# Kernel tuning notes

Measured on AMD Instinct MI355X. Metric: run time of the kernel, lower is better.

## Reference

```python
import jax, jax.numpy as jnp
import numpy as np

HIDDEN = 1024
HEADS = 16
HEAD = HIDDEN // HEADS
B, S = 2, 2048


def setup_inputs() -> dict:
    key = jax.random.key(0)
    ks = jax.random.split(key, 8)
    query = jax.random.normal(ks[0], (B, S, HIDDEN), dtype=jnp.float32)
    key_t = jax.random.normal(ks[1], (B, S, HIDDEN), dtype=jnp.float32)
    value = jax.random.normal(ks[2], (B, S, HIDDEN), dtype=jnp.float32)
    # causal mask, broadcastable over batch and heads; 0 -> masked (-inf)
    mask = jnp.tril(jnp.ones((S, S), dtype=jnp.int32))[None, None, :, :]
    # torch Linear weights are [out_features, in_features]
    scale = 0.02
    Wq = jax.random.normal(ks[3], (HIDDEN, HIDDEN), dtype=jnp.float32) * scale
    Wk = jax.random.normal(ks[4], (HIDDEN, HIDDEN), dtype=jnp.float32) * scale
    Wv = jax.random.normal(ks[5], (HIDDEN, HIDDEN), dtype=jnp.float32) * scale
    Wo = jax.random.normal(ks[6], (HIDDEN, HIDDEN), dtype=jnp.float32) * scale
    bo = jax.random.normal(ks[7], (HIDDEN,), dtype=jnp.float32) * scale
    return {"query": query, "key": key_t, "value": value, "mask": mask,
            "Wq": Wq, "Wk": Wk, "Wv": Wv, "Wo": Wo, "bo": bo}


def reference(query, key, value, mask, Wq, Wk, Wv, Wo, bo):
    b = query.shape[0]
    # Linear (no bias): x @ W^T, then split into heads -> [b, h, s, d]
    def heads(x, W):
        y = jnp.einsum('bse,oe->bso', x, W)
        return y.reshape(b, -1, HEADS, HEAD).transpose(0, 2, 1, 3)
    Q = heads(query, Wq)
    K = heads(key, Wk)
    V = heads(value, Wv)
    inv_scale = 1.0 / jnp.sqrt(jnp.float32(HEAD))
    scores = jnp.einsum('bhqd,bhkd->bhqk', Q, K) * inv_scale  # [b,h,s,s]
    scores = jnp.where(mask == 0, -jnp.inf, scores)
    attn = jax.nn.softmax(scores, axis=-1)
    x = jnp.einsum('bhqk,bhkd->bhqd', attn, V)
    x = x.transpose(0, 2, 1, 3).reshape(b, -1, HIDDEN)
    return jnp.einsum('bse,oe->bso', x, Wo) + bo
```

## Files before the change

kernel.cpp:

```cpp
#include <hip/hip_runtime.h>


typedef __attribute__((ext_vector_type(8))) short short8;
typedef __attribute__((ext_vector_type(4))) float f32x4;
typedef unsigned int u32;
typedef unsigned short u16;

__device__ inline f32x4 mfma16(short8 a, short8 b, f32x4 c) {
    return __builtin_amdgcn_mfma_f32_16x16x32_bf16(a, b, c, 0, 0, 0);
}
__device__ inline u16 f2bf(float f) {
    union { float f; u32 u; } v; v.f = f;
    u32 r = v.u + 0x7fff + ((v.u >> 16) & 1);
    return (u16)(r >> 16);
}
__device__ inline void gll16(void* lds, const void* g) {
    __builtin_amdgcn_global_load_lds((const __attribute__((address_space(1))) u32*)g,
                                     (__attribute__((address_space(3))) u32*)lds,
                                     16, 0, 0);
}
__device__ inline u32 pkbf(float hi, float lo) {
    return __builtin_amdgcn_perm(__float_as_uint(hi), __float_as_uint(lo),
                                 0x07060302u);
}

__global__ __launch_bounds__(256)
void cvt_all(const float* __restrict__ q, const float* __restrict__ k,
             const float* __restrict__ v, const float* __restrict__ wq,
             const float* __restrict__ wk, const float* __restrict__ wv,
             const float* __restrict__ wo,
             u16* __restrict__ q16, u16* __restrict__ k16,
             u16* __restrict__ v16, u16* __restrict__ w16) {
    const size_t QKV = 1u << 22;
    const size_t WSZ = 1u << 20;
    size_t base = ((size_t)blockIdx.x * 256 + threadIdx.x) * 8;
    const float* src; u16* dst; size_t off; float scale = 1.0f;
    if (base < QKV)            { src = q; dst = q16; off = base;
                                 scale = 0.125f * 1.44269504f; }
    else if (base < 2 * QKV)   { src = k; dst = k16; off = base - QKV;     }
    else if (base < 3 * QKV)   { src = v; dst = v16; off = base - 2 * QKV; }
    else {
        size_t wb = base - 3 * QKV;
        int wi = (int)(wb >> 20); off = wb & (WSZ - 1);
        src = wi == 0 ? wq : wi == 1 ? wk : wi == 2 ? wv : wo;
        dst = w16 + (size_t)wi * WSZ;
    }
    float4 f0 = *(const float4*)(src + off);
    float4 f1 = *(const float4*)(src + off + 4);
    short8 s = { (short)f2bf(f0.x * scale), (short)f2bf(f0.y * scale),
                 (short)f2bf(f0.z * scale), (short)f2bf(f0.w * scale),
                 (short)f2bf(f1.x * scale), (short)f2bf(f1.y * scale),
                 (short)f2bf(f1.z * scale), (short)f2bf(f1.w * scale) };
    *(short8*)(dst + off) = s;
}

__global__ __launch_bounds__(256)
void gemm_qkv(const u16* __restrict__ q16, const u16* __restrict__ k16,
              const u16* __restrict__ v16, const u16* __restrict__ w16,
              u16* __restrict__ Qg, u16* __restrict__ Kg, u16* __restrict__ Vt) {
    const int K = 1024;
    __shared__ u16 As[2][128 * 32];
    __shared__ u16 Bs[2][128 * 32];
    const int z = blockIdx.z;
    const u16* A = z == 0 ? q16 : z == 1 ? k16 : v16;
    const u16* W = w16 + (size_t)z * (1u << 20);

    const int tid = threadIdx.x, lane = tid & 63, w = tid >> 6;
    const int ln15 = lane & 15, quad = lane >> 4;
    const int fr = (ln15 >> 1) & 3;
    const int lrow = lane >> 2;
    const int lcs = (((lane & 3) ^ ((lane >> 3) & 3)) << 3);
    const int m0 = blockIdx.y * 128, n0 = blockIdx.x * 128;
    const int wm = (w >> 1) * 64, wn = (w & 1) * 64;

    f32x4 acc[4][4] = {};

    #pragma unroll
    for (int c = 0; c < 2; ++c) {
        gll16(&As[0][(w * 32 + c * 16) * 32],
              &A[(size_t)(m0 + w * 32 + c * 16 + lrow) * K + lcs]);
        gll16(&Bs[0][(w * 32 + c * 16) * 32],
              &W[(size_t)(n0 + w * 32 + c * 16 + lrow) * K + lcs]);
    }

    for (int i = 0; i < 32; ++i) {
        const int cur = i & 1, nb = cur ^ 1;
        __asm__ volatile("s_waitcnt vmcnt(0)" ::: "memory");
        __builtin_amdgcn_s_barrier();
        __builtin_amdgcn_sched_barrier(0);

        if (i < 31) {
            const int k0 = (i + 1) * 32;
            #pragma unroll
            for (int c = 0; c < 2; ++c) {
                gll16(&As[nb][(w * 32 + c * 16) * 32],
                      &A[(size_t)(m0 + w * 32 + c * 16 + lrow) * K + k0 + lcs]);
                gll16(&Bs[nb][(w * 32 + c * 16) * 32],
                      &W[(size_t)(n0 + w * 32 + c * 16 + lrow) * K + k0 + lcs]);
            }
        }
        __builtin_amdgcn_sched_barrier(0);

        short8 a[4], b[4];
        #pragma unroll
        for (int mt = 0; mt < 4; ++mt)
            a[mt] = *(const short8*)&As[cur][(wm + mt * 16 + ln15) * 32 +
                                            ((quad ^ fr) << 3)];
        #pragma unroll
        for (int nt = 0; nt < 4; ++nt)
            b[nt] = *(const short8*)&Bs[cur][(wn + nt * 16 + ln15) * 32 +
                                            ((quad ^ fr) << 3)];
        #pragma unroll
        for (int mt = 0; mt < 4; ++mt)
            #pragma unroll
            for (int nt = 0; nt < 4; ++nt)
                acc[mt][nt] = mfma16(a[mt], b[nt], acc[mt][nt]);
    }

    #pragma unroll
    for (int mt = 0; mt < 4; ++mt)
        #pragma unroll
        for (int nt = 0; nt < 4; ++nt)
            #pragma unroll
            for (int r = 0; r < 4; ++r) {
                int m = m0 + wm + mt * 16 + quad * 4 + r;
                int n = n0 + wn + nt * 16 + ln15;
                u16 hv = f2bf(acc[mt][nt][r]);
                if (z == 2) {
                    int b_ = m >> 11, s_ = m & 2047, h_ = n >> 6, d_ = n & 63;
                    int kl = s_ & 63;
                    int sp = (s_ & ~63) + (kl & 15) * 4 + (kl >> 4);
                    Vt[((size_t)(b_ * 16 + h_) * 64 + d_) * 2048 + sp] = hv;
                } else {
                    u16* dst = z ? Kg : Qg;
                    dst[(size_t)m * 1024 + n] = hv;
                }
            }
}

__global__ __launch_bounds__(256)
void gemm_out(const u16* __restrict__ A, const u16* __restrict__ W,
              const float* __restrict__ bias, float* __restrict__ out) {
    const int K = 1024;
    __shared__ u16 As[2][64 * 64];
    __shared__ u16 Bs[2][128 * 64];
    const int id = blockIdx.x;
    const int by = id >> 3, bx = id & 7;

    const int tid = threadIdx.x, lane = tid & 63, w = tid >> 6;
    const int ln15 = lane & 15, quad = lane >> 4, s7 = ln15 & 7;
    const int lr = lane >> 3;
    const int lcs = (((lane & 7) ^ lr) << 3);
    const int m0 = by * 64, n0 = bx * 128;
    const int wm = (w & 1) * 32, wn = (w >> 1) * 64;

    f32x4 acc[2][4] = {};

    #pragma unroll
    for (int c = 0; c < 2; ++c)
        gll16(&As[0][(w * 16 + c * 8) * 64],
              &A[(size_t)(m0 + w * 16 + c * 8 + lr) * K + lcs]);
    #pragma unroll
    for (int c = 0; c < 4; ++c)
        gll16(&Bs[0][(w * 32 + c * 8) * 64],
              &W[(size_t)(n0 + w * 32 + c * 8 + lr) * K + lcs]);

    for (int i = 0; i < 16; ++i) {
        const int cur = i & 1, nb = cur ^ 1;
        __asm__ volatile("s_waitcnt vmcnt(0)" ::: "memory");
        __builtin_amdgcn_s_barrier();
        __builtin_amdgcn_sched_barrier(0);

        if (i < 15) {
            const int k0 = (i + 1) * 64;
            #pragma unroll
            for (int c = 0; c < 2; ++c)
                gll16(&As[nb][(w * 16 + c * 8) * 64],
                      &A[(size_t)(m0 + w * 16 + c * 8 + lr) * K + k0 + lcs]);
            #pragma unroll
            for (int c = 0; c < 4; ++c)
                gll16(&Bs[nb][(w * 32 + c * 8) * 64],
                      &W[(size_t)(n0 + w * 32 + c * 8 + lr) * K + k0 + lcs]);
        }
        __builtin_amdgcn_sched_barrier(0);

        #pragma unroll
        for (int kh = 0; kh < 2; ++kh) {
            short8 a[2], b[4];
            #pragma unroll
            for (int mt = 0; mt < 2; ++mt)
                a[mt] = *(const short8*)&As[cur][(wm + mt * 16 + ln15) * 64 +
                                                (((kh * 4 + quad) ^ s7) << 3)];
            #pragma unroll
            for (int nt = 0; nt < 4; ++nt)
                b[nt] = *(const short8*)&Bs[cur][(wn + nt * 16 + ln15) * 64 +
                                                (((kh * 4 + quad) ^ s7) << 3)];
            #pragma unroll
            for (int mt = 0; mt < 2; ++mt)
                #pragma unroll
                for (int nt = 0; nt < 4; ++nt)
                    acc[mt][nt] = mfma16(a[mt], b[nt], acc[mt][nt]);
        }
    }

    #pragma unroll
    for (int mt = 0; mt < 2; ++mt)
        #pragma unroll
        for (int nt = 0; nt < 4; ++nt)
            #pragma unroll
            for (int r = 0; r < 4; ++r) {
                int m = m0 + wm + mt * 16 + quad * 4 + r;
                int n = n0 + wn + nt * 16 + ln15;
                out[(size_t)m * 1024 + n] = acc[mt][nt][r] + bias[n];
            }
}

__global__ __launch_bounds__(256)
void attn3(const u16* __restrict__ Qg, const u16* __restrict__ Kg,
           const u16* __restrict__ Vt, u16* __restrict__ Xb) {
    __shared__ u16 Kl[2][64 * 64];
    __shared__ u16 Vl[2][64 * 64];
    __shared__ u16 Pl[4][16 * 72];

    const int id = blockIdx.x;
    const int bh = id & 31, qt = 31 - (id >> 5);
    const int b = bh >> 4, h = bh & 15;
    const int tid = threadIdx.x, lane = tid & 63, w = tid >> 6;
    const int ln15 = lane & 15, quad = lane >> 4, s7 = ln15 & 7;
    const int lr = lane >> 3;
    const int lcs = (((lane & 7) ^ lr) << 3);
    const u16* Kbase = Kg + (size_t)b * 2048 * 1024 + h * 64;
    const u16* Vbase = Vt + (size_t)bh * 64 * 2048;
    const float M0L = 8.65617025f;
    const int q0 = qt * 64;

    const u16* qrow = Qg + (size_t)(b * 2048 + q0 + w * 16 + ln15) * 1024 + h * 64;
    short8 aq0 = *(const short8*)(qrow + quad * 8);
    short8 aq1 = *(const short8*)(qrow + 32 + quad * 8);
    __asm__ volatile("s_waitcnt vmcnt(0)" ::: "memory");

    f32x4 o[4] = {};
    float lsum[4] = {0.f, 0.f, 0.f, 0.f};

    #pragma unroll
    for (int c = 0; c < 2; ++c) {
        const int r0 = w * 16 + c * 8;
        gll16(&Kl[0][r0 * 64], Kbase + (size_t)(r0 + lr) * 1024 + lcs);
        gll16(&Vl[0][r0 * 64], Vbase + (size_t)(r0 + lr) * 2048 + lcs);
    }

    for (int kt = 0; kt <= qt; ++kt) {
        const int cur = kt & 1, nb = cur ^ 1;
        __asm__ volatile("s_waitcnt vmcnt(0)" ::: "memory");
        __builtin_amdgcn_s_barrier();
        __builtin_amdgcn_sched_barrier(0);

        if (kt < qt) {
            const int nk = (kt + 1) * 64;
            #pragma unroll
            for (int c = 0; c < 2; ++c) {
                const int r0 = w * 16 + c * 8;
                gll16(&Kl[nb][r0 * 64], Kbase + (size_t)(nk + r0 + lr) * 1024 + lcs);
                gll16(&Vl[nb][r0 * 64], Vbase + (size_t)(r0 + lr) * 2048 + nk + lcs);
            }
        }
        __builtin_amdgcn_sched_barrier(0);

        f32x4 sc[4];
        #pragma unroll
        for (int ct = 0; ct < 4; ++ct) {
            short8 b0 = *(const short8*)&Kl[cur][(ct * 16 + ln15) * 64 +
                                                ((quad ^ s7) << 3)];
            short8 b1 = *(const short8*)&Kl[cur][(ct * 16 + ln15) * 64 +
                                                (((4 + quad) ^ s7) << 3)];
            f32x4 c = {};
            c = mfma16(aq0, b0, c);
            c = mfma16(aq1, b1, c);
            sc[ct] = c;
        }

        const bool diag = (kt == qt);
        #pragma unroll
        for (int r = 0; r < 4; ++r) {
            float s0 = sc[0][r], s1 = sc[1][r], s2 = sc[2][r], s3 = sc[3][r];
            if (diag) {
                const int qq = w * 16 + quad * 4 + r;
                s0 = (ln15      <= qq) ? s0 : -1e30f;
                s1 = (16 + ln15 <= qq) ? s1 : -1e30f;
                s2 = (32 + ln15 <= qq) ? s2 : -1e30f;
                s3 = (48 + ln15 <= qq) ? s3 : -1e30f;
            }
            float p0 = __builtin_amdgcn_exp2f(s0 - M0L);
            float p1 = __builtin_amdgcn_exp2f(s1 - M0L);
            float p2 = __builtin_amdgcn_exp2f(s2 - M0L);
            float p3 = __builtin_amdgcn_exp2f(s3 - M0L);
            uint2 pw = make_uint2(pkbf(p1, p0), pkbf(p3, p2));
            *(uint2*)&Pl[w][(quad * 4 + r) * 72 + ln15 * 4] = pw;
            lsum[r] += (p0 + p1) + (p2 + p3);
        }

        __asm__ volatile("s_waitcnt lgkmcnt(0)" ::: "memory");
        short8 ap0 = *(const short8*)&Pl[w][ln15 * 72 + quad * 8];
        short8 ap1 = *(const short8*)&Pl[w][ln15 * 72 + 32 + quad * 8];

        #pragma unroll
        for (int dt = 0; dt < 4; ++dt) {
            short8 bv0 = *(const short8*)&Vl[cur][(dt * 16 + ln15) * 64 +
                                                 ((quad ^ s7) << 3)];
            short8 bv1 = *(const short8*)&Vl[cur][(dt * 16 + ln15) * 64 +
                                                 (((4 + quad) ^ s7) << 3)];
            o[dt] = mfma16(ap0, bv0, o[dt]);
            o[dt] = mfma16(ap1, bv1, o[dt]);
        }
    }

    #pragma unroll
    for (int r = 0; r < 4; ++r) {
        float l = lsum[r];
        #pragma unroll
        for (int off = 1; off < 16; off <<= 1)
            l += __shfl_xor(l, off);
        lsum[r] = l;
    }
    #pragma unroll
    for (int dt = 0; dt < 4; ++dt)
        #pragma unroll
        for (int r = 0; r < 4; ++r) {
            int q = q0 + w * 16 + quad * 4 + r;
            Xb[(size_t)(b * 2048 + q) * 1024 + h * 64 + dt * 16 + ln15] =
                f2bf(o[dt][r] / lsum[r]);
        }
}

extern "C" void kernel_launch(void* const* d_in, const int* in_sizes, int n_in,
                              void* d_out, int out_size, void* d_ws, size_t ws_size,
                              hipStream_t stream) {
    const float* query = (const float*)d_in[0];
    const float* key   = (const float*)d_in[1];
    const float* value = (const float*)d_in[2];
    const float* Wq = (const float*)d_in[4];
    const float* Wk = (const float*)d_in[5];
    const float* Wv = (const float*)d_in[6];
    const float* Wo = (const float*)d_in[7];
    const float* bo = (const float*)d_in[8];
    float* out = (float*)d_out;

    u16* ws  = (u16*)d_ws;
    const size_t T = 1ull << 22;
    u16* q16 = ws;
    u16* k16 = ws + T;
    u16* v16 = ws + 2 * T;
    u16* w16 = ws + 3 * T;
    u16* Qg  = ws + 4 * T;
    u16* Kg  = ws + 5 * T;
    u16* Vt  = (u16*)d_out;
    u16* Xb  = q16;
    const size_t WSZ = 1ull << 20;

    cvt_all<<<8192, 256, 0, stream>>>(query, key, value, Wq, Wk, Wv, Wo,
                                      q16, k16, v16, w16);

    gemm_qkv<<<dim3(8, 32, 3), 256, 0, stream>>>(q16, k16, v16, w16, Qg, Kg, Vt);

    attn3<<<1024, 256, 0, stream>>>(Qg, Kg, Vt, Xb);

    gemm_out<<<512, 256, 0, stream>>>(Xb, w16 + 3 * WSZ, bo, out);
}
```

Baseline: 222.5 us.

## Triple-buffer LDS tiles in QKV, output GEMM and attention kernels

Switches the LDS staging in all three main kernels from double to triple buffering with prefetch distance two. The wait changes from vmcnt(0) to a partial vmcnt, so only the current tile's loads must finish before the barrier while the next tile's loads stay in flight. The intent is to hide more global-load latency behind the MFMA work. It costs 50% more LDS for the K/V and A/B tiles, which may reduce occupancy, and adds ring-index bookkeeping.

Measured after the change: 223.3 us. About the same (+0.3%).

```diff
diff --git a/kernel.cpp b/kernel.cpp
--- a/kernel.cpp
+++ b/kernel.cpp
@@ -59,8 +59,8 @@
               const u16* __restrict__ v16, const u16* __restrict__ w16,
               u16* __restrict__ Qg, u16* __restrict__ Kg, u16* __restrict__ Vt) {
     const int K = 1024;
-    __shared__ u16 As[2][128 * 32];
-    __shared__ u16 Bs[2][128 * 32];
+    __shared__ u16 As[3][128 * 32];
+    __shared__ u16 Bs[3][128 * 32];
     const int z = blockIdx.z;
     const u16* A = z == 0 ? q16 : z == 1 ? k16 : v16;
     const u16* W = w16 + (size_t)z * (1u << 20);
@@ -76,21 +76,28 @@
     f32x4 acc[4][4] = {};
 
     #pragma unroll
-    for (int c = 0; c < 2; ++c) {
-        gll16(&As[0][(w * 32 + c * 16) * 32],
-              &A[(size_t)(m0 + w * 32 + c * 16 + lrow) * K + lcs]);
-        gll16(&Bs[0][(w * 32 + c * 16) * 32],
-              &W[(size_t)(n0 + w * 32 + c * 16 + lrow) * K + lcs]);
-    }
-
-    for (int i = 0; i < 32; ++i) {
-        const int cur = i & 1, nb = cur ^ 1;
-        __asm__ volatile("s_waitcnt vmcnt(0)" ::: "memory");
+    for (int t = 0; t < 2; ++t)
+        #pragma unroll
+        for (int c = 0; c < 2; ++c) {
+            gll16(&As[t][(w * 32 + c * 16) * 32],
+                  &A[(size_t)(m0 + w * 32 + c * 16 + lrow) * K + t * 32 + lcs]);
+            gll16(&Bs[t][(w * 32 + c * 16) * 32],
+                  &W[(size_t)(n0 + w * 32 + c * 16 + lrow) * K + t * 32 + lcs]);
+        }
+
+    int cur = 0;
+    for (int t = 0; t < 32; ++t) {
+        if (t < 31) {
+            __asm__ volatile("s_waitcnt vmcnt(4)" ::: "memory");
+        } else {
+            __asm__ volatile("s_waitcnt vmcnt(0)" ::: "memory");
+        }
         __builtin_amdgcn_s_barrier();
         __builtin_amdgcn_sched_barrier(0);
 
-        if (i < 31) {
-            const int k0 = (i + 1) * 32;
+        if (t < 30) {
+            const int k0 = (t + 2) * 32;
+            const int nb = (cur + 2 >= 3) ? cur - 1 : cur + 2;
             #pragma unroll
             for (int c = 0; c < 2; ++c) {
                 gll16(&As[nb][(w * 32 + c * 16) * 32],
@@ -115,6 +122,8 @@
             #pragma unroll
             for (int nt = 0; nt < 4; ++nt)
                 acc[mt][nt] = mfma16(a[mt], b[nt], acc[mt][nt]);
+
+        cur = (cur == 2) ? 0 : cur + 1;
     }
 
     #pragma unroll
@@ -142,8 +151,8 @@
 void gemm_out(const u16* __restrict__ A, const u16* __restrict__ W,
               const float* __restrict__ bias, float* __restrict__ out) {
     const int K = 1024;
-    __shared__ u16 As[2][64 * 64];
-    __shared__ u16 Bs[2][128 * 64];
+    __shared__ u16 As[3][64 * 64];
+    __shared__ u16 Bs[3][128 * 64];
     const int id = blockIdx.x;
     const int by = id >> 3, bx = id & 7;
 
@@ -157,22 +166,30 @@
     f32x4 acc[2][4] = {};
 
     #pragma unroll
-    for (int c = 0; c < 2; ++c)
-        gll16(&As[0][(w * 16 + c * 8) * 64],
-              &A[(size_t)(m0 + w * 16 + c * 8 + lr) * K + lcs]);
-    #pragma unroll
-    for (int c = 0; c < 4; ++c)
-        gll16(&Bs[0][(w * 32 + c * 8) * 64],
-              &W[(size_t)(n0 + w * 32 + c * 8 + lr) * K + lcs]);
-
+    for (int t = 0; t < 2; ++t) {
+        #pragma unroll
+        for (int c = 0; c < 2; ++c)
+            gll16(&As[t][(w * 16 + c * 8) * 64],
+                  &A[(size_t)(m0 + w * 16 + c * 8 + lr) * K + t * 64 + lcs]);
+        #pragma unroll
+        for (int c = 0; c < 4; ++c)
+            gll16(&Bs[t][(w * 32 + c * 8) * 64],
+                  &W[(size_t)(n0 + w * 32 + c * 8 + lr) * K + t * 64 + lcs]);
+    }
+
+    int cur = 0;
     for (int i = 0; i < 16; ++i) {
-        const int cur = i & 1, nb = cur ^ 1;
-        __asm__ volatile("s_waitcnt vmcnt(0)" ::: "memory");
+        if (i < 15) {
+            __asm__ volatile("s_waitcnt vmcnt(6)" ::: "memory");
+        } else {
+            __asm__ volatile("s_waitcnt vmcnt(0)" ::: "memory");
+        }
         __builtin_amdgcn_s_barrier();
         __builtin_amdgcn_sched_barrier(0);
 
-        if (i < 15) {
-            const int k0 = (i + 1) * 64;
+        if (i < 14) {
+            const int k0 = (i + 2) * 64;
+            const int nb = (cur + 2 >= 3) ? cur - 1 : cur + 2;
             #pragma unroll
             for (int c = 0; c < 2; ++c)
                 gll16(&As[nb][(w * 16 + c * 8) * 64],
@@ -201,6 +218,7 @@
                 for (int nt = 0; nt < 4; ++nt)
                     acc[mt][nt] = mfma16(a[mt], b[nt], acc[mt][nt]);
         }
+        cur = (cur == 2) ? 0 : cur + 1;
     }
 
     #pragma unroll
@@ -218,8 +236,8 @@
 __global__ __launch_bounds__(256)
 void attn3(const u16* __restrict__ Qg, const u16* __restrict__ Kg,
            const u16* __restrict__ Vt, u16* __restrict__ Xb) {
-    __shared__ u16 Kl[2][64 * 64];
-    __shared__ u16 Vl[2][64 * 64];
+    __shared__ u16 Kl[3][64 * 64];
+    __shared__ u16 Vl[3][64 * 64];
     __shared__ u16 Pl[4][16 * 72];
 
     const int id = blockIdx.x;
@@ -248,15 +266,28 @@
         gll16(&Kl[0][r0 * 64], Kbase + (size_t)(r0 + lr) * 1024 + lcs);
         gll16(&Vl[0][r0 * 64], Vbase + (size_t)(r0 + lr) * 2048 + lcs);
     }
-
+    if (qt >= 1) {
+        #pragma unroll
+        for (int c = 0; c < 2; ++c) {
+            const int r0 = w * 16 + c * 8;
+            gll16(&Kl[1][r0 * 64], Kbase + (size_t)(64 + r0 + lr) * 1024 + lcs);
+            gll16(&Vl[1][r0 * 64], Vbase + (size_t)(r0 + lr) * 2048 + 64 + lcs);
+        }
+    }
+
+    int cur = 0;
     for (int kt = 0; kt <= qt; ++kt) {
-        const int cur = kt & 1, nb = cur ^ 1;
-        __asm__ volatile("s_waitcnt vmcnt(0)" ::: "memory");
+        if (kt < qt) {
+            __asm__ volatile("s_waitcnt vmcnt(4)" ::: "memory");
+        } else {
+            __asm__ volatile("s_waitcnt vmcnt(0)" ::: "memory");
+        }
         __builtin_amdgcn_s_barrier();
         __builtin_amdgcn_sched_barrier(0);
 
-        if (kt < qt) {
-            const int nk = (kt + 1) * 64;
+        if (kt + 2 <= qt) {
+            const int nk = (kt + 2) * 64;
+            const int nb = (cur + 2 >= 3) ? cur - 1 : cur + 2;
             #pragma unroll
             for (int c = 0; c < 2; ++c) {
                 const int r0 = w * 16 + c * 8;
@@ -312,6 +343,7 @@
             o[dt] = mfma16(ap0, bv0, o[dt]);
             o[dt] = mfma16(ap1, bv1, o[dt]);
         }
+        cur = (cur == 2) ? 0 : cur + 1;
     }
 
     #pragma unroll
```
